# Kernel tuning notes

Measured on AMD Instinct MI355X. Metric: run time of the kernel, lower is better.

The kernel has to match this reference:

```python
import jax, jax.numpy as jnp
import numpy as np

B, Z, U, P, X, H = 16, 64, 8, 128, 64, 128  # batch, z_dim, u_dim, phi_dim, x_dim, hid_dim


def _glorot(key, fan_in, fan_out):
    return jax.random.normal(key, (fan_in, fan_out), dtype=jnp.float32) * np.sqrt(2.0 / (fan_in + fan_out)).astype(np.float32)


def setup_inputs() -> dict:
    key = jax.random.key(0)
    ks = jax.random.split(key, 8)
    return {
        "x": jax.random.normal(ks[0], (B, X), dtype=jnp.float32),
        "Linv": jax.random.normal(ks[1], (B, Z, U, P, P), dtype=jnp.float32) * 0.02,
        "Q": jax.random.normal(ks[2], (B, Z, U, 1, P), dtype=jnp.float32),
        "W1": _glorot(ks[3], X, H), "b1": jnp.zeros((H,), jnp.float32),
        "W2": _glorot(ks[4], H, H), "b2": jnp.zeros((H,), jnp.float32),
        "W3": _glorot(ks[5], H, H), "b3": jnp.zeros((H,), jnp.float32),
        "W4": _glorot(ks[6], H, P), "b4": jnp.zeros((P,), jnp.float32),
        "logSigEps": jnp.log(jnp.full((U,), 0.1, dtype=jnp.float32)),
    }


def _encoder(x, W1, b1, W2, b2, W3, b3, W4, b4):
    h = jax.nn.elu(x @ W1 + b1)
    h = jax.nn.elu(h @ W2 + b2)
    h = jax.nn.elu(h @ W3 + b3)
    return h @ W4 + b4  # [B, P]


def reference(x, Linv, Q, W1, b1, W2, b2, W3, b3, W4, b4, logSigEps):
    phi = _encoder(x, W1, b1, W2, b2, W3, b3, W4, b4)  # [B, P]
    Q2 = Q[..., 0, :]  # [B, Z, U, P]
    # K = (Q @ Linv^T).squeeze(-2): K[b,z,u,q] = sum_p Q[b,z,u,p] * Linv[b,z,u,q,p]
    K = jnp.einsum("bzup,bzuqp->bzuq", Q2, Linv)
    # mu = K @ phi  -> [B, Z, U, 1]
    mu = jnp.einsum("bzuq,bq->bzu", K, phi)[..., None]
    # sigma_scale = 1 + phi^T Linv phi -> [B, Z, U]
    sigma_scale = 1.0 + jnp.einsum("bp,bzupq,bq->bzu", phi, Linv, phi)
    pred_cov_diag = jnp.exp(logSigEps) * sigma_scale  # [B, Z, U]
    return (mu, pred_cov_diag)
```

## Files before the change

### kernel.cpp

```cpp
#include <hip/hip_runtime.h>

#define B 16
#define Z 64
#define U 8
#define P 128
#define X 64
#define H 128
#define BZU (B * Z * U)
#define BLOCKS 256
#define THREADS 1024
#define M_PER_BLOCK (BZU / BLOCKS)
#define M_PER_WAVE 2

typedef float f32x4 __attribute__((ext_vector_type(4)));

__device__ __forceinline__ float elu1(float v) {
    return v > 0.0f ? v : (expf(v) - 1.0f);
}

__global__ __launch_bounds__(THREADS, 4) void fused_kernel(
    const float* __restrict__ x,
    const float* __restrict__ Linv,
    const float* __restrict__ Q,
    const float* __restrict__ W1, const float* __restrict__ b1,
    const float* __restrict__ W2, const float* __restrict__ b2,
    const float* __restrict__ W3, const float* __restrict__ b3,
    const float* __restrict__ W4, const float* __restrict__ b4,
    const float* __restrict__ logSigEps,
    float* __restrict__ out_mu,
    float* __restrict__ out_cov)
{
    __shared__ float xs[X];
    __shared__ float hs[H];
    __shared__ float ps[8][H];
    __shared__ float phis[P];

    const int blk  = blockIdx.x;
    const int t    = threadIdx.x;
    const int b    = blk >> 4;
    const int j    = t & (H - 1);
    const int sl   = t >> 7;
    const int wave = t >> 6;
    const int lane = t & 63;
    const int j4   = (lane & 31) * 4;
    const int r0   = lane >> 5;

    if (t < X) xs[t] = x[b * X + t];
    __syncthreads();

    {
        float v = 0.0f; const int k0 = sl * 8;
        #pragma unroll
        for (int k = k0; k < k0 + 8; ++k) v = fmaf(xs[k], W1[k * H + j], v);
        ps[sl][j] = v;
    }
    __syncthreads();
    if (t < H) {
        float v = b1[j];
        #pragma unroll
        for (int s = 0; s < 8; ++s) v += ps[s][j];
        hs[j] = elu1(v);
    }
    __syncthreads();

    {
        float v = 0.0f; const int k0 = sl * 16;
        #pragma unroll
        for (int k = k0; k < k0 + 16; ++k) v = fmaf(hs[k], W2[k * H + j], v);
        ps[sl][j] = v;
    }
    __syncthreads();
    if (t < H) {
        float v = b2[j];
        #pragma unroll
        for (int s = 0; s < 8; ++s) v += ps[s][j];
        hs[j] = elu1(v);
    }
    __syncthreads();

    {
        float v = 0.0f; const int k0 = sl * 16;
        #pragma unroll
        for (int k = k0; k < k0 + 16; ++k) v = fmaf(hs[k], W3[k * H + j], v);
        ps[sl][j] = v;
    }
    __syncthreads();
    if (t < H) {
        float v = b3[j];
        #pragma unroll
        for (int s = 0; s < 8; ++s) v += ps[s][j];
        hs[j] = elu1(v);
    }
    __syncthreads();

    {
        float v = 0.0f; const int k0 = sl * 16;
        #pragma unroll
        for (int k = k0; k < k0 + 16; ++k) v = fmaf(hs[k], W4[k * P + j], v);
        ps[sl][j] = v;
    }
    __syncthreads();
    if (t < H) {
        float v = b4[j];
        #pragma unroll
        for (int s = 0; s < 8; ++s) v += ps[s][j];
        phis[j] = v;
    }
    __syncthreads();

    const float pp0 = phis[j4 + 0], pp1 = phis[j4 + 1],
                pp2 = phis[j4 + 2], pp3 = phis[j4 + 3];

    #pragma unroll
    for (int i = 0; i < M_PER_WAVE; ++i) {
        const int m = blk * M_PER_BLOCK + wave * M_PER_WAVE + i;
        const float4 qv = *(const float4*)(Q + (size_t)m * P + j4);
        const f32x4* __restrict__ Lp =
            (const f32x4*)Linv + (size_t)m * (P * P / 4);

        float mu = 0.0f, sg = 0.0f;
        #pragma unroll
        for (int c = 0; c < 4; ++c) {
            f32x4 Lb[16];
            #pragma unroll
            for (int k2 = 0; k2 < 16; ++k2)
                Lb[k2] = __builtin_nontemporal_load(Lp + lane + 64 * (16 * c + k2));
            float pi[16];
            #pragma unroll
            for (int k2 = 0; k2 < 16; ++k2) pi[k2] = phis[r0 + 32 * c + 2 * k2];
            #pragma unroll
            for (int k2 = 0; k2 < 16; ++k2) {
                const f32x4 L = Lb[k2];
                const float dq = L[0] * qv.x + L[1] * qv.y + L[2] * qv.z + L[3] * qv.w;
                const float dp = L[0] * pp0 + L[1] * pp1 + L[2] * pp2 + L[3] * pp3;
                mu = fmaf(pi[k2], dq, mu);
                sg = fmaf(pi[k2], dp, sg);
            }
        }

        #pragma unroll
        for (int off = 32; off > 0; off >>= 1) {
            mu += __shfl_down(mu, off, 64);
            sg += __shfl_down(sg, off, 64);
        }
        if (lane == 0) {
            out_mu[m]  = mu;
            out_cov[m] = expf(logSigEps[m & (U - 1)]) * (1.0f + sg);
        }
    }
}

extern "C" void kernel_launch(void* const* d_in, const int* in_sizes, int n_in,
                              void* d_out, int out_size, void* d_ws, size_t ws_size,
                              hipStream_t stream) {
    const float* x        = (const float*)d_in[0];
    const float* Linv     = (const float*)d_in[1];
    const float* Q        = (const float*)d_in[2];
    const float* W1       = (const float*)d_in[3];
    const float* b1       = (const float*)d_in[4];
    const float* W2       = (const float*)d_in[5];
    const float* b2       = (const float*)d_in[6];
    const float* W3       = (const float*)d_in[7];
    const float* b3       = (const float*)d_in[8];
    const float* W4       = (const float*)d_in[9];
    const float* b4       = (const float*)d_in[10];
    const float* logSigEps= (const float*)d_in[11];

    float* out_mu  = (float*)d_out;
    float* out_cov = (float*)d_out + BZU;

    fused_kernel<<<BLOCKS, THREADS, 0, stream>>>(
        x, Linv, Q, W1, b1, W2, b2, W3, b3, W4, b4, logSigEps,
        out_mu, out_cov);
}
```

Baseline: 88.53 us.

## Prefetch MLP weights into registers and double-buffer Linv streaming across matrices

Loads all encoder weight slices into registers at kernel start so their global latency overlaps, instead of being paid serially between barriers. Replaces the per-matrix chunked Linv loop with a two-buffer software pipeline across both matrices a wave owns, issuing the next chunk's loads before the current chunk is consumed. This is meant to hide memory latency in the bandwidth-bound Linv stream. In exchange it raises register pressure (56 weight floats plus 16 vector buffers), which could spill or lower occupancy at 1024 threads per block.

```diff
diff --git a/kernel.cpp b/kernel.cpp
--- a/kernel.cpp
+++ b/kernel.cpp
@@ -44,14 +44,30 @@
     const int lane = t & 63;
     const int j4   = (lane & 31) * 4;
     const int r0   = lane >> 5;
-
-    if (t < X) xs[t] = x[b * X + t];
-    __syncthreads();
-
-    {
-        float v = 0.0f; const int k0 = sl * 8;
-        #pragma unroll
-        for (int k = k0; k < k0 + 8; ++k) v = fmaf(xs[k], W1[k * H + j], v);
+    const int m0   = blk * M_PER_BLOCK + wave * M_PER_WAVE;
+
+    float xv = 0.0f;
+    if (t < X) xv = x[b * X + t];
+
+    const int k1 = sl * 8;
+    const int k0 = sl * 16;
+    float w1r[8], w2r[16], w3r[16], w4r[16];
+    #pragma unroll
+    for (int e = 0; e < 8; ++e)  w1r[e] = W1[(k1 + e) * H + j];
+    #pragma unroll
+    for (int e = 0; e < 16; ++e) w2r[e] = W2[(k0 + e) * H + j];
+    #pragma unroll
+    for (int e = 0; e < 16; ++e) w3r[e] = W3[(k0 + e) * H + j];
+    #pragma unroll
+    for (int e = 0; e < 16; ++e) w4r[e] = W4[(k0 + e) * P + j];
+
+    if (t < X) xs[t] = xv;
+    __syncthreads();
+
+    {
+        float v = 0.0f;
+        #pragma unroll
+        for (int e = 0; e < 8; ++e) v = fmaf(xs[k1 + e], w1r[e], v);
         ps[sl][j] = v;
     }
     __syncthreads();
@@ -64,9 +80,9 @@
     __syncthreads();
 
     {
-        float v = 0.0f; const int k0 = sl * 16;
-        #pragma unroll
-        for (int k = k0; k < k0 + 16; ++k) v = fmaf(hs[k], W2[k * H + j], v);
+        float v = 0.0f;
+        #pragma unroll
+        for (int e = 0; e < 16; ++e) v = fmaf(hs[k0 + e], w2r[e], v);
         ps[sl][j] = v;
     }
     __syncthreads();
@@ -79,9 +95,9 @@
     __syncthreads();
 
     {
-        float v = 0.0f; const int k0 = sl * 16;
-        #pragma unroll
-        for (int k = k0; k < k0 + 16; ++k) v = fmaf(hs[k], W3[k * H + j], v);
+        float v = 0.0f;
+        #pragma unroll
+        for (int e = 0; e < 16; ++e) v = fmaf(hs[k0 + e], w3r[e], v);
         ps[sl][j] = v;
     }
     __syncthreads();
@@ -94,9 +110,9 @@
     __syncthreads();
 
     {
-        float v = 0.0f; const int k0 = sl * 16;
-        #pragma unroll
-        for (int k = k0; k < k0 + 16; ++k) v = fmaf(hs[k], W4[k * P + j], v);
+        float v = 0.0f;
+        #pragma unroll
+        for (int e = 0; e < 16; ++e) v = fmaf(hs[k0 + e], w4r[e], v);
         ps[sl][j] = v;
     }
     __syncthreads();
@@ -111,42 +127,73 @@
     const float pp0 = phis[j4 + 0], pp1 = phis[j4 + 1],
                 pp2 = phis[j4 + 2], pp3 = phis[j4 + 3];
 
-    #pragma unroll
-    for (int i = 0; i < M_PER_WAVE; ++i) {
-        const int m = blk * M_PER_BLOCK + wave * M_PER_WAVE + i;
-        const float4 qv = *(const float4*)(Q + (size_t)m * P + j4);
-        const f32x4* __restrict__ Lp =
-            (const f32x4*)Linv + (size_t)m * (P * P / 4);
-
-        float mu = 0.0f, sg = 0.0f;
-        #pragma unroll
-        for (int c = 0; c < 4; ++c) {
-            f32x4 Lb[16];
+    const f32x4* __restrict__ Lp0 =
+        (const f32x4*)Linv + (size_t)m0 * (P * P / 4);
+    const f32x4* __restrict__ Lp1 = Lp0 + (P * P / 4);
+    const float4 qv0 = *(const float4*)(Q + (size_t)m0 * P + j4);
+    const float4 qv1 = *(const float4*)(Q + (size_t)(m0 + 1) * P + j4);
+
+    f32x4 bufA[8], bufB[8];
+
+    #pragma unroll
+    for (int e = 0; e < 8; ++e)
+        bufA[e] = __builtin_nontemporal_load(Lp0 + lane + 64 * e);
+    #pragma unroll
+    for (int e = 0; e < 8; ++e)
+        bufB[e] = __builtin_nontemporal_load(Lp0 + lane + 64 * (8 + e));
+
+    float mu = 0.0f, sg = 0.0f;
+    #pragma unroll
+    for (int g = 0; g < 16; ++g) {
+        f32x4* cur = (g & 1) ? bufB : bufA;
+        const float qx = (g < 8) ? qv0.x : qv1.x;
+        const float qy = (g < 8) ? qv0.y : qv1.y;
+        const float qz = (g < 8) ? qv0.z : qv1.z;
+        const float qw = (g < 8) ? qv0.w : qv1.w;
+        const int gg = g & 7;
+
+        #pragma unroll
+        for (int e = 0; e < 8; ++e) {
+            const f32x4 L = cur[e];
+            const float pi = phis[r0 + 16 * gg + 2 * e];
+            const float dq = L[0] * qx + L[1] * qy + L[2] * qz + L[3] * qw;
+            const float dp = L[0] * pp0 + L[1] * pp1 + L[2] * pp2 + L[3] * pp3;
+            mu = fmaf(pi, dq, mu);
+            sg = fmaf(pi, dp, sg);
+        }
+
+        if (g < 14) {
+            const int gn = g + 2;
+            const f32x4* __restrict__ Lp = (gn < 8) ? Lp0 : Lp1;
+            const int gh = gn & 7;
             #pragma unroll
-            for (int k2 = 0; k2 < 16; ++k2)
-                Lb[k2] = __builtin_nontemporal_load(Lp + lane + 64 * (16 * c + k2));
-            float pi[16];
+            for (int e = 0; e < 8; ++e)
+                cur[e] = __builtin_nontemporal_load(Lp + lane + 64 * (8 * gh + e));
+        }
+
+        if (g == 7) {
             #pragma unroll
-            for (int k2 = 0; k2 < 16; ++k2) pi[k2] = phis[r0 + 32 * c + 2 * k2];
-            #pragma unroll
-            for (int k2 = 0; k2 < 16; ++k2) {
-                const f32x4 L = Lb[k2];
-                const float dq = L[0] * qv.x + L[1] * qv.y + L[2] * qv.z + L[3] * qv.w;
-                const float dp = L[0] * pp0 + L[1] * pp1 + L[2] * pp2 + L[3] * pp3;
-                mu = fmaf(pi[k2], dq, mu);
-                sg = fmaf(pi[k2], dp, sg);
+            for (int off = 32; off > 0; off >>= 1) {
+                mu += __shfl_down(mu, off, 64);
+                sg += __shfl_down(sg, off, 64);
             }
+            if (lane == 0) {
+                out_mu[m0]  = mu;
+                out_cov[m0] = expf(logSigEps[m0 & (U - 1)]) * (1.0f + sg);
+            }
+            mu = 0.0f; sg = 0.0f;
         }
-
-        #pragma unroll
-        for (int off = 32; off > 0; off >>= 1) {
-            mu += __shfl_down(mu, off, 64);
-            sg += __shfl_down(sg, off, 64);
-        }
-        if (lane == 0) {
-            out_mu[m]  = mu;
-            out_cov[m] = expf(logSigEps[m & (U - 1)]) * (1.0f + sg);
-        }
+    }
+
+    #pragma unroll
+    for (int off = 32; off > 0; off >>= 1) {
+        mu += __shfl_down(mu, off, 64);
+        sg += __shfl_down(sg, off, 64);
+    }
+    if (lane == 0) {
+        const int m = m0 + 1;
+        out_mu[m]  = mu;
+        out_cov[m] = expf(logSigEps[m & (U - 1)]) * (1.0f + sg);
     }
 }
 
```

New measurement: 88.31 us. About the same (-0.3%).
